# Performance work log

Hardware: AMD Instinct MI355X
Metric: run time of the kernel (lower is better)

The kernel has to match this reference:

```python
import jax, jax.numpy as jnp
import numpy as np

N, E, D = 50000, 600000, 128


def setup_inputs() -> dict:
    key = jax.random.key(0)
    ks = jax.random.split(key, 7)
    s = 1.0 / np.sqrt(D)
    return {
        "x": jax.random.normal(ks[0], (N, D), dtype=jnp.float32),
        "edge_index": jax.random.randint(ks[1], (2, E), 0, N, dtype=jnp.int64),
        "Wl1": jax.random.normal(ks[2], (D, D), dtype=jnp.float32) * s,
        "Wr1": jax.random.normal(ks[3], (D, D), dtype=jnp.float32) * s,
        "b1": jnp.zeros((D,), dtype=jnp.float32),
        "Wl2": jax.random.normal(ks[4], (D, D), dtype=jnp.float32) * s,
        "Wr2": jax.random.normal(ks[5], (D, D), dtype=jnp.float32) * s,
        "b2": jnp.zeros((D,), dtype=jnp.float32),
    }


def _sage_conv(h, edge_index, Wl, Wr, b):
    # PyG SAGEConv (mean aggr): out = lin_l(mean_{j in N(i)} h_j) + lin_r(h_i)
    src, dst = edge_index[0], edge_index[1]
    n = h.shape[0]
    msg = h[src]                                            # [E, D] gather
    agg = jax.ops.segment_sum(msg, dst, num_segments=n)     # [N, D] scatter-add
    cnt = jax.ops.segment_sum(jnp.ones((src.shape[0],), h.dtype), dst,
                              num_segments=n)               # in-degree
    agg = agg / jnp.maximum(cnt, 1.0)[:, None]              # mean (0 for isolated)
    return agg @ Wl + h @ Wr + b


def reference(x, edge_index, Wl1, Wr1, b1, Wl2, Wr2, b2):
    h = jax.nn.relu(_sage_conv(x, edge_index, Wl1, Wr1, b1))
    # F.dropout(p=0.5) is identity in eval mode (deterministic baseline)
    return _sage_conv(h, edge_index, Wl2, Wr2, b2)
```

## Files before the change

### kernel.cpp

```cpp
#include <hip/hip_runtime.h>

typedef unsigned int u32;
typedef unsigned short u16;
typedef __attribute__((ext_vector_type(8))) short bf16x8;
typedef __attribute__((ext_vector_type(4))) float f32x4;

__device__ __forceinline__ u32 f2bf(float f) {
  u32 x = __float_as_uint(f);
  return (x + 0x7fffu + ((x >> 16) & 1u)) >> 16;
}
__device__ __forceinline__ float bf2f(u16 u) {
  return __uint_as_float(((u32)u) << 16);
}
__device__ __forceinline__ void addbf8(float* a, uint4 v) {
  a[0] += bf2f((u16)v.x); a[1] += bf2f((u16)(v.x >> 16));
  a[2] += bf2f((u16)v.y); a[3] += bf2f((u16)(v.y >> 16));
  a[4] += bf2f((u16)v.z); a[5] += bf2f((u16)(v.z >> 16));
  a[6] += bf2f((u16)v.w); a[7] += bf2f((u16)(v.w >> 16));
}

__global__ void setup_kernel(const float* __restrict__ Wl1, const float* __restrict__ Wr1,
                             const float* __restrict__ Wl2, const float* __restrict__ Wr2,
                             u16* __restrict__ G1, u16* __restrict__ G2,
                             int* __restrict__ cnt, int n) {
  int b = blockIdx.x;
  if (b < 256) {
    const float* Wl = (b < 128) ? Wl1 : Wl2;
    const float* Wr = (b < 128) ? Wr1 : Wr2;
    u16* G = (b < 128) ? G1 : G2;
    int id = (b & 127) * 256 + threadIdx.x;
    int c = id >> 7;
    int k = id & 127;
    const float* W = (c < 128) ? Wl : Wr;
    float v = W[k * 128 + (c & 127)];
    G[c * 128 + (k ^ ((c & 7) << 3))] = (u16)f2bf(v);
  } else {
    int i = (b - 256) * 256 + threadIdx.x;
    if (i < n) cnt[i] = 0;
  }
}

__global__ void hist_kernel(const int* __restrict__ dst, int* __restrict__ cnt,
                            int* __restrict__ pos, int E) {
  int e = blockIdx.x * blockDim.x + threadIdx.x;
  if (e < E) pos[e] = atomicAdd(&cnt[dst[e]], 1);
}

#define SCAN_CHUNK 2048

__global__ __launch_bounds__(256) void scan_sums(const int* __restrict__ cnt,
                                                 int* __restrict__ bsum, int n) {
  __shared__ int red[256];
  int t = threadIdx.x;
  int base = blockIdx.x * SCAN_CHUNK + t * 8;
  int s = 0;
#pragma unroll
  for (int i = 0; i < 8; ++i) {
    int idx = base + i;
    if (idx < n) s += cnt[idx];
  }
  red[t] = s;
  __syncthreads();
  for (int off = 128; off > 0; off >>= 1) {
    if (t < off) red[t] += red[t + off];
    __syncthreads();
  }
  if (t == 0) bsum[blockIdx.x] = red[0];
}

__global__ __launch_bounds__(256) void scan_apply(
    const int* __restrict__ cnt, const int* __restrict__ bsum, int nb,
    int* __restrict__ row_ptr, float* __restrict__ inv_cnt, int n) {
  __shared__ int sc[256];
  __shared__ int base_s;
  int t = threadIdx.x;
  if (t == 0) {
    int run = 0;
    int bid = blockIdx.x;
    int base = 0;
    for (int i = 0; i < nb; ++i) {
      if (i == bid) base = run;
      run += bsum[i];
    }
    base_s = base;
    if (bid == 0) row_ptr[n] = run;
  }
  int chunk_base = blockIdx.x * SCAN_CHUNK + t * 8;
  int v[8];
  int s = 0;
#pragma unroll
  for (int i = 0; i < 8; ++i) {
    int idx = chunk_base + i;
    v[i] = (idx < n) ? cnt[idx] : 0;
    s += v[i];
  }
  sc[t] = s;
  __syncthreads();
  for (int off = 1; off < 256; off <<= 1) {
    int add = (t >= off) ? sc[t - off] : 0;
    __syncthreads();
    sc[t] += add;
    __syncthreads();
  }
  int run = base_s + ((t > 0) ? sc[t - 1] : 0);
#pragma unroll
  for (int i = 0; i < 8; ++i) {
    int idx = chunk_base + i;
    if (idx < n) {
      row_ptr[idx] = run;
      inv_cnt[idx] = 1.0f / (float)max(v[i], 1);
      run += v[i];
    }
  }
}

template <int IN_BF16>
__device__ __forceinline__ void gemm_tiles(const void* in_, const u16* __restrict__ G,
                                           const float* __restrict__ bias,
                                           u16* __restrict__ yl, u16* __restrict__ yr,
                                           int n, uint4* lds4, int gb) {
  char* As = (char*)lds4;
  char* Bt = (char*)lds4 + 16384;
  const int t = threadIdx.x;
  const int lane = t & 63;
  const int wave = t >> 6;
  const int wr = wave >> 1;
  const int wc = wave & 1;
  const int lhi = lane >> 4;
  const int llo = lane & 15;

  {
    const char* gbp = (const char*)G;
#pragma unroll
    for (int i = 0; i < 16; ++i) {
      int g = i * 256 + t;
      __builtin_amdgcn_global_load_lds((const u32*)(gbp + g * 16),
                                       (u32*)(Bt + g * 16), 16, 0, 0);
    }
  }

  const int ntiles = (n + 63) / 64;
#pragma unroll 1
  for (int tile = gb * 2; tile < ntiles && tile < gb * 2 + 2; ++tile) {
    const int row0 = tile * 64;
    __syncthreads();
#pragma unroll
    for (int i = 0; i < 4; ++i) {
      int g = t + i * 256;
      int r = g >> 4;
      int gcl = g & 15;
      int row = row0 + r;
      if (IN_BF16) {
        if (row < n) {
          int gcs = gcl ^ (r & 7);
          __builtin_amdgcn_global_load_lds(
              (const u32*)((const u16*)in_ + (size_t)row * 128 + gcs * 8),
              (u32*)(As + g * 16), 16, 0, 0);
        } else {
          uint4 z = {0u, 0u, 0u, 0u};
          *(uint4*)(As + g * 16) = z;
        }
      } else {
        uint4 pk = {0u, 0u, 0u, 0u};
        if (row < n) {
          const float4* pp = (const float4*)((const float*)in_ + (size_t)row * 128 + gcl * 8);
          float4 v0 = pp[0], v1 = pp[1];
          pk.x = f2bf(v0.x) | (f2bf(v0.y) << 16);
          pk.y = f2bf(v0.z) | (f2bf(v0.w) << 16);
          pk.z = f2bf(v1.x) | (f2bf(v1.y) << 16);
          pk.w = f2bf(v1.z) | (f2bf(v1.w) << 16);
        }
        *(uint4*)(As + r * 256 + ((gcl * 16) ^ ((r & 7) << 4))) = pk;
      }
    }
    __syncthreads();

    f32x4 acc[2][8];
#pragma unroll
    for (int fr = 0; fr < 2; ++fr)
#pragma unroll
      for (int fc = 0; fc < 8; ++fc) acc[fr][fc] = {0.f, 0.f, 0.f, 0.f};

#pragma unroll
    for (int ks = 0; ks < 4; ++ks) {
      const int kbyte = ks * 64 + lhi * 16;
      bf16x8 a[2], bb[8];
#pragma unroll
      for (int fr = 0; fr < 2; ++fr) {
        int r = wr * 32 + fr * 16 + llo;
        a[fr] = *(const bf16x8*)(As + r * 256 + (kbyte ^ ((r & 7) << 4)));
      }
#pragma unroll
      for (int fc = 0; fc < 8; ++fc) {
        int c = wc * 128 + fc * 16 + llo;
        bb[fc] = *(const bf16x8*)(Bt + c * 256 + (kbyte ^ ((c & 7) << 4)));
      }
#pragma unroll
      for (int fr = 0; fr < 2; ++fr)
#pragma unroll
        for (int fc = 0; fc < 8; ++fc)
          acc[fr][fc] = __builtin_amdgcn_mfma_f32_16x16x32_bf16(a[fr], bb[fc], acc[fr][fc], 0, 0, 0);
    }

#pragma unroll 1
    for (int ph = 0; ph < 2; ++ph) {
      __syncthreads();
      if (wc == ph) {
#pragma unroll
        for (int fc = 0; fc < 8; ++fc) {
          int cc = fc * 16 + llo;
          float bv = (ph == 1) ? bias[cc] : 0.0f;
#pragma unroll
          for (int fr = 0; fr < 2; ++fr) {
#pragma unroll
            for (int i = 0; i < 4; ++i) {
              int row = wr * 32 + fr * 16 + lhi * 4 + i;
              *(u16*)(As + row * 256 + ((cc * 2) ^ (lhi << 5))) =
                  (u16)f2bf(acc[fr][fc][i] + bv);
            }
          }
        }
      }
      __syncthreads();
      u16* outp = (ph == 0) ? yl : yr;
#pragma unroll
      for (int j = 0; j < 4; ++j) {
        int idx = t + j * 256;
        int row = idx >> 4;
        int cb = (idx & 15) * 16;
        int grow = row0 + row;
        if (grow < n) {
          uint4 v = *(const uint4*)(As + row * 256 + (cb ^ (((row >> 2) & 3) << 5)));
          *(uint4*)((char*)(outp + (size_t)grow * 128) + cb) = v;
        }
      }
    }
  }
}

__global__ __launch_bounds__(256, 2) void gemm1_fill_kernel(
    const float* __restrict__ x, const u16* __restrict__ G1, const float* __restrict__ b1,
    u16* __restrict__ yl, u16* __restrict__ yr, int n,
    const int* __restrict__ src, const int* __restrict__ dst,
    const int* __restrict__ pos, const int* __restrict__ row_ptr,
    int* __restrict__ colv, int E, int GB) {
  __shared__ uint4 lds4[5120];
  if ((int)blockIdx.x < GB) {
    gemm_tiles<0>(x, G1, b1, yl, yr, n, lds4, blockIdx.x);
  } else {
    int base = ((int)blockIdx.x - GB) * 2048 + threadIdx.x;
    int dd[8], pp[8], ss[8], rp[8];
#pragma unroll
    for (int j = 0; j < 8; ++j) {
      int e = base + j * 256;
      if (e < E) { dd[j] = dst[e]; pp[j] = pos[e]; ss[j] = src[e]; }
    }
#pragma unroll
    for (int j = 0; j < 8; ++j) {
      int e = base + j * 256;
      if (e < E) rp[j] = row_ptr[dd[j]];
    }
#pragma unroll
    for (int j = 0; j < 8; ++j) {
      int e = base + j * 256;
      if (e < E) colv[rp[j] + pp[j]] = ss[j];
    }
  }
}

template <int IN_BF16>
__global__ __launch_bounds__(256, 2) void gemm_kernel(
    const void* __restrict__ in_, const u16* __restrict__ G, const float* __restrict__ bias,
    u16* __restrict__ yl, u16* __restrict__ yr, int n) {
  __shared__ uint4 lds4[5120];
  gemm_tiles<IN_BF16>(in_, G, bias, yl, yr, n, lds4, blockIdx.x);
}

template <int RELU, int OUT_BF16>
__global__ __launch_bounds__(256) void agg_kernel(
    const u16* __restrict__ yl, const u16* __restrict__ yr,
    const int* __restrict__ row_ptr, const int* __restrict__ colv,
    const float* __restrict__ invc, void* __restrict__ out_, int n) {
  int node = blockIdx.x * 16 + (threadIdx.x >> 4);
  if (node >= n) return;
  int sl = threadIdx.x & 15;
  int beg = row_ptr[node], end = row_ptr[node + 1];
  uint4 rv = *(const uint4*)(yr + (size_t)node * 128 + sl * 8);
  float s = invc[node];
  float a[8] = {0.f, 0.f, 0.f, 0.f, 0.f, 0.f, 0.f, 0.f};
  for (int e0 = beg; e0 < end; e0 += 8) {
    int m = end - e0;
    if (m > 8) m = 8;
    uint4 v0, v1, v2, v3, v4, v5, v6, v7;
    if (0 < m) v0 = *(const uint4*)(yl + (size_t)colv[e0 + 0] * 128 + sl * 8);
    if (1 < m) v1 = *(const uint4*)(yl + (size_t)colv[e0 + 1] * 128 + sl * 8);
    if (2 < m) v2 = *(const uint4*)(yl + (size_t)colv[e0 + 2] * 128 + sl * 8);
    if (3 < m) v3 = *(const uint4*)(yl + (size_t)colv[e0 + 3] * 128 + sl * 8);
    if (4 < m) v4 = *(const uint4*)(yl + (size_t)colv[e0 + 4] * 128 + sl * 8);
    if (5 < m) v5 = *(const uint4*)(yl + (size_t)colv[e0 + 5] * 128 + sl * 8);
    if (6 < m) v6 = *(const uint4*)(yl + (size_t)colv[e0 + 6] * 128 + sl * 8);
    if (7 < m) v7 = *(const uint4*)(yl + (size_t)colv[e0 + 7] * 128 + sl * 8);
    if (0 < m) addbf8(a, v0);
    if (1 < m) addbf8(a, v1);
    if (2 < m) addbf8(a, v2);
    if (3 < m) addbf8(a, v3);
    if (4 < m) addbf8(a, v4);
    if (5 < m) addbf8(a, v5);
    if (6 < m) addbf8(a, v6);
    if (7 < m) addbf8(a, v7);
  }
  float r[8];
  r[0] = bf2f((u16)rv.x); r[1] = bf2f((u16)(rv.x >> 16));
  r[2] = bf2f((u16)rv.y); r[3] = bf2f((u16)(rv.y >> 16));
  r[4] = bf2f((u16)rv.z); r[5] = bf2f((u16)(rv.z >> 16));
  r[6] = bf2f((u16)rv.w); r[7] = bf2f((u16)(rv.w >> 16));
  float o[8];
#pragma unroll
  for (int j = 0; j < 8; ++j) {
    o[j] = a[j] * s + r[j];
    if (RELU) o[j] = fmaxf(o[j], 0.f);
  }
  if (OUT_BF16) {
    uint4 pk;
    pk.x = f2bf(o[0]) | (f2bf(o[1]) << 16);
    pk.y = f2bf(o[2]) | (f2bf(o[3]) << 16);
    pk.z = f2bf(o[4]) | (f2bf(o[5]) << 16);
    pk.w = f2bf(o[6]) | (f2bf(o[7]) << 16);
    *(uint4*)((u16*)out_ + (size_t)node * 128 + sl * 8) = pk;
  } else {
    float4 q0 = {o[0], o[1], o[2], o[3]};
    float4 q1 = {o[4], o[5], o[6], o[7]};
    float* op = (float*)out_ + (size_t)node * 128 + sl * 8;
    *(float4*)op = q0;
    *(float4*)(op + 4) = q1;
  }
}

extern "C" void kernel_launch(void* const* d_in, const int* in_sizes, int n_in,
                              void* d_out, int out_size, void* d_ws, size_t ws_size,
                              hipStream_t stream) {
  const float* x = (const float*)d_in[0];
  const int* ei = (const int*)d_in[1];
  const float* Wl1 = (const float*)d_in[2];
  const float* Wr1 = (const float*)d_in[3];
  const float* b1 = (const float*)d_in[4];
  const float* Wl2 = (const float*)d_in[5];
  const float* Wr2 = (const float*)d_in[6];
  const float* b2 = (const float*)d_in[7];

  const int N = in_sizes[0] / 128;
  const int E = in_sizes[1] / 2;
  const int* srcv = ei;
  const int* dstv = ei + E;

  char* ws = (char*)d_ws;
  u16* yl = (u16*)ws;       ws += (size_t)N * 128 * 2;
  u16* yr = (u16*)ws;       ws += (size_t)N * 128 * 2;
  u16* hbf = (u16*)ws;      ws += (size_t)N * 128 * 2;
  u16* G1 = (u16*)ws;       ws += 256 * 128 * 2;
  u16* G2 = (u16*)ws;       ws += 256 * 128 * 2;
  int* colv = (int*)ws;     ws += (size_t)E * 4;
  int* pos = (int*)ws;      ws += (size_t)E * 4;
  int* row_ptr = (int*)ws;  ws += ((size_t)N + 64) * 4;
  int* cnt = (int*)ws;      ws += (size_t)N * 4;
  float* invc = (float*)ws; ws += (size_t)N * 4;
  int* bsum = (int*)ws;     ws += 256 * 4;

  const int nsb = (N + SCAN_CHUNK - 1) / SCAN_CHUNK;
  const int ntiles = (N + 63) / 64;
  const int GB = (ntiles + 1) / 2;
  const int FB = (E + 2047) / 2048;

  setup_kernel<<<256 + (N + 255) / 256, 256, 0, stream>>>(Wl1, Wr1, Wl2, Wr2, G1, G2, cnt, N);
  hist_kernel<<<(E + 255) / 256, 256, 0, stream>>>(dstv, cnt, pos, E);
  scan_sums<<<nsb, 256, 0, stream>>>(cnt, bsum, N);
  scan_apply<<<nsb, 256, 0, stream>>>(cnt, bsum, nsb, row_ptr, invc, N);
  gemm1_fill_kernel<<<GB + FB, 256, 0, stream>>>(x, G1, b1, yl, yr, N,
                                                 srcv, dstv, pos, row_ptr, colv, E, GB);
  agg_kernel<1, 1><<<(N + 15) / 16, 256, 0, stream>>>(yl, yr, row_ptr, colv, invc, hbf, N);
  gemm_kernel<1><<<GB, 256, 0, stream>>>(hbf, G2, b2, yl, yr, N);
  agg_kernel<0, 0><<<(N + 15) / 16, 256, 0, stream>>>(yl, yr, row_ptr, colv, invc, d_out, N);
}
```

Measured before the change: 139.1 us.

## Overlap degree histogram with first GEMM and merge scan into one kernel

Moves the atomic in-degree histogram into the same launch as the first-layer GEMM, so the histogram blocks run alongside GEMM tiles. The CSR column fill then becomes its own kernel after the scan. The two-pass scan is replaced by one kernel in which each block recomputes its prefix base by summing all earlier counts. This drops the bsum buffer and one launch, at the cost of redundant reads of cnt that grow with block index.

```diff
diff --git a/kernel.cpp b/kernel.cpp
--- a/kernel.cpp
+++ b/kernel.cpp
@@ -40,52 +40,31 @@
   }
 }
 
-__global__ void hist_kernel(const int* __restrict__ dst, int* __restrict__ cnt,
-                            int* __restrict__ pos, int E) {
-  int e = blockIdx.x * blockDim.x + threadIdx.x;
-  if (e < E) pos[e] = atomicAdd(&cnt[dst[e]], 1);
-}
-
 #define SCAN_CHUNK 2048
 
-__global__ __launch_bounds__(256) void scan_sums(const int* __restrict__ cnt,
-                                                 int* __restrict__ bsum, int n) {
-  __shared__ int red[256];
+__global__ __launch_bounds__(256) void scan_kernel(
+    const int* __restrict__ cnt, int* __restrict__ row_ptr,
+    float* __restrict__ inv_cnt, int n, int nsb) {
+  __shared__ int sc[256];
+  __shared__ int base_sh;
   int t = threadIdx.x;
-  int base = blockIdx.x * SCAN_CHUNK + t * 8;
-  int s = 0;
-#pragma unroll
-  for (int i = 0; i < 8; ++i) {
-    int idx = base + i;
-    if (idx < n) s += cnt[idx];
-  }
-  red[t] = s;
+  int bid = blockIdx.x;
+  int lim = bid * SCAN_CHUNK;
+  if (lim > n) lim = n;
+  int ps = 0;
+#pragma unroll 4
+  for (int i = t; i < lim; i += 256) ps += cnt[i];
+  sc[t] = ps;
   __syncthreads();
   for (int off = 128; off > 0; off >>= 1) {
-    if (t < off) red[t] += red[t + off];
-    __syncthreads();
-  }
-  if (t == 0) bsum[blockIdx.x] = red[0];
-}
-
-__global__ __launch_bounds__(256) void scan_apply(
-    const int* __restrict__ cnt, const int* __restrict__ bsum, int nb,
-    int* __restrict__ row_ptr, float* __restrict__ inv_cnt, int n) {
-  __shared__ int sc[256];
-  __shared__ int base_s;
-  int t = threadIdx.x;
-  if (t == 0) {
-    int run = 0;
-    int bid = blockIdx.x;
-    int base = 0;
-    for (int i = 0; i < nb; ++i) {
-      if (i == bid) base = run;
-      run += bsum[i];
-    }
-    base_s = base;
-    if (bid == 0) row_ptr[n] = run;
-  }
-  int chunk_base = blockIdx.x * SCAN_CHUNK + t * 8;
+    if (t < off) sc[t] += sc[t + off];
+    __syncthreads();
+  }
+  if (t == 0) base_sh = sc[0];
+  __syncthreads();
+  int base = base_sh;
+  __syncthreads();
+  int chunk_base = bid * SCAN_CHUNK + t * 8;
   int v[8];
   int s = 0;
 #pragma unroll
@@ -102,7 +81,7 @@
     sc[t] += add;
     __syncthreads();
   }
-  int run = base_s + ((t > 0) ? sc[t - 1] : 0);
+  int run = base + sc[t] - s;
 #pragma unroll
   for (int i = 0; i < 8; ++i) {
     int idx = chunk_base + i;
@@ -112,6 +91,7 @@
       run += v[i];
     }
   }
+  if (bid == nsb - 1 && t == 255) row_ptr[n] = base + sc[255];
 }
 
 template <int IN_BF16>
@@ -238,33 +218,40 @@
   }
 }
 
-__global__ __launch_bounds__(256, 2) void gemm1_fill_kernel(
+__global__ __launch_bounds__(256, 2) void gemm1_hist_kernel(
     const float* __restrict__ x, const u16* __restrict__ G1, const float* __restrict__ b1,
     u16* __restrict__ yl, u16* __restrict__ yr, int n,
-    const int* __restrict__ src, const int* __restrict__ dst,
-    const int* __restrict__ pos, const int* __restrict__ row_ptr,
-    int* __restrict__ colv, int E, int GB) {
+    const int* __restrict__ dst, int* __restrict__ cnt, int* __restrict__ pos,
+    int E, int GB) {
   __shared__ uint4 lds4[5120];
   if ((int)blockIdx.x < GB) {
     gemm_tiles<0>(x, G1, b1, yl, yr, n, lds4, blockIdx.x);
   } else {
-    int base = ((int)blockIdx.x - GB) * 2048 + threadIdx.x;
-    int dd[8], pp[8], ss[8], rp[8];
-#pragma unroll
-    for (int j = 0; j < 8; ++j) {
-      int e = base + j * 256;
-      if (e < E) { dd[j] = dst[e]; pp[j] = pos[e]; ss[j] = src[e]; }
-    }
-#pragma unroll
-    for (int j = 0; j < 8; ++j) {
-      int e = base + j * 256;
-      if (e < E) rp[j] = row_ptr[dd[j]];
-    }
-#pragma unroll
-    for (int j = 0; j < 8; ++j) {
-      int e = base + j * 256;
-      if (e < E) colv[rp[j] + pp[j]] = ss[j];
-    }
+    int e = ((int)blockIdx.x - GB) * 256 + threadIdx.x;
+    if (e < E) pos[e] = atomicAdd(&cnt[dst[e]], 1);
+  }
+}
+
+__global__ __launch_bounds__(256) void fill_kernel(
+    const int* __restrict__ src, const int* __restrict__ dst,
+    const int* __restrict__ pos, const int* __restrict__ row_ptr,
+    int* __restrict__ colv, int E) {
+  int base = blockIdx.x * 2048 + threadIdx.x;
+  int dd[8], pp[8], ss[8], rp[8];
+#pragma unroll
+  for (int j = 0; j < 8; ++j) {
+    int e = base + j * 256;
+    if (e < E) { dd[j] = dst[e]; pp[j] = pos[e]; ss[j] = src[e]; }
+  }
+#pragma unroll
+  for (int j = 0; j < 8; ++j) {
+    int e = base + j * 256;
+    if (e < E) rp[j] = row_ptr[dd[j]];
+  }
+#pragma unroll
+  for (int j = 0; j < 8; ++j) {
+    int e = base + j * 256;
+    if (e < E) colv[rp[j] + pp[j]] = ss[j];
   }
 }
 
@@ -364,19 +351,18 @@
   int* row_ptr = (int*)ws;  ws += ((size_t)N + 64) * 4;
   int* cnt = (int*)ws;      ws += (size_t)N * 4;
   float* invc = (float*)ws; ws += (size_t)N * 4;
-  int* bsum = (int*)ws;     ws += 256 * 4;
 
   const int nsb = (N + SCAN_CHUNK - 1) / SCAN_CHUNK;
   const int ntiles = (N + 63) / 64;
   const int GB = (ntiles + 1) / 2;
+  const int HB = (E + 255) / 256;
   const int FB = (E + 2047) / 2048;
 
   setup_kernel<<<256 + (N + 255) / 256, 256, 0, stream>>>(Wl1, Wr1, Wl2, Wr2, G1, G2, cnt, N);
-  hist_kernel<<<(E + 255) / 256, 256, 0, stream>>>(dstv, cnt, pos, E);
-  scan_sums<<<nsb, 256, 0, stream>>>(cnt, bsum, N);
-  scan_apply<<<nsb, 256, 0, stream>>>(cnt, bsum, nsb, row_ptr, invc, N);
-  gemm1_fill_kernel<<<GB + FB, 256, 0, stream>>>(x, G1, b1, yl, yr, N,
-                                                 srcv, dstv, pos, row_ptr, colv, E, GB);
+  gemm1_hist_kernel<<<GB + HB, 256, 0, stream>>>(x, G1, b1, yl, yr, N,
+                                                 dstv, cnt, pos, E, GB);
+  scan_kernel<<<nsb, 256, 0, stream>>>(cnt, row_ptr, invc, N, nsb);
+  fill_kernel<<<FB, 256, 0, stream>>>(srcv, dstv, pos, row_ptr, colv, E);
   agg_kernel<1, 1><<<(N + 15) / 16, 256, 0, stream>>>(yl, yr, row_ptr, colv, invc, hbf, N);
   gemm_kernel<1><<<GB, 256, 0, stream>>>(hbf, G2, b2, yl, yr, N);
   agg_kernel<0, 0><<<(N + 15) / 16, 256, 0, stream>>>(yl, yr, row_ptr, colv, invc, d_out, N);
```

Measured after the change: 140.1 us. Within noise of the previous version (+0.7%).
